# Kernel optimization log

Measured on AMD Instinct MI355X. Metric: run time of the kernel, lower is better.

## Reference

```python
import jax, jax.numpy as jnp
import numpy as np

RANK = 16
ALPHA = 32.0
SCALING = ALPHA / RANK  # 2.0


def setup_inputs() -> dict:
    key = jax.random.key(0)
    k1, k2, k3, k4, k5 = jax.random.split(key, 5)
    B, S, D_IN, D_OUT = 4, 4096, 4096, 4096
    x = jax.random.normal(k1, (B, S, D_IN), dtype=jnp.float32)
    W = jax.random.normal(k2, (D_OUT, D_IN), dtype=jnp.float32) * 0.02
    b = jax.random.normal(k3, (D_OUT,), dtype=jnp.float32) * 0.02
    lora_A = jax.random.normal(k4, (RANK, D_IN), dtype=jnp.float32) * 0.02
    lora_B = jax.random.normal(k5, (D_OUT, RANK), dtype=jnp.float32) * 0.02
    return {"x": x, "W": W, "b": b, "lora_A": lora_A, "lora_B": lora_B}


def reference(x, W, b, lora_A, lora_B):
    # Base linear: y = x @ W^T + b
    base = jnp.einsum("bsd,od->bso", x, W) + b
    # LoRA delta: mathematically x @ (B @ A)^T * scaling == ((x @ A^T) @ B^T) * scaling.
    # We chain the two small rank-limited GEMMs (same math, efficient form).
    xa = jnp.einsum("bsd,rd->bsr", x, lora_A)           # [B,S,rank]
    lora_out = jnp.einsum("bsr,or->bso", xa, lora_B)    # [B,S,out]
    return base + SCALING * lora_out
```

## Files before the change

### kernel.cpp

```cpp
#include <hip/hip_runtime.h>
#include <hip/hip_bf16.h>
#include <cstdint>

constexpr int  KDIM  = 4096;
constexpr int  NDIM  = 4096;
constexpr long MDIM  = 16384;
constexpr int  RANK_ = 16;
constexpr float SCALE_ = 2.0f;

constexpr int BK = 64;
constexpr int NT = KDIM / BK;

using bf16x8 = __attribute__((ext_vector_type(8))) short;
using f32x4  = __attribute__((ext_vector_type(4))) float;

__device__ __forceinline__ void gload_lds16(const void* g, void* l) {
  __builtin_amdgcn_global_load_lds(
      (const __attribute__((address_space(1))) void*)g,
      (__attribute__((address_space(3))) void*)l, 16, 0, 0);
}

__device__ __forceinline__ unsigned short f2bf(float f) {
  union { float f; unsigned u; } v; v.f = f;
  unsigned r = v.u + 0x7FFFu + ((v.u >> 16) & 1u);
  return (unsigned short)(r >> 16);
}

__global__ __launch_bounds__(256) void prep_w_kernel(
    const float* __restrict__ W, const float* __restrict__ lA,
    const float* __restrict__ lB, unsigned short* __restrict__ Wp) {
  const long total8 = (long)NDIM * KDIM / 8;
  for (long t = blockIdx.x * (long)blockDim.x + threadIdx.x; t < total8;
       t += (long)gridDim.x * blockDim.x) {
    const int o  = (int)(t / (KDIM / 8));
    const int d8 = (int)(t % (KDIM / 8)) * 8;
    const float4* w4 = reinterpret_cast<const float4*>(W + (size_t)o * KDIM + d8);
    float4 w0 = w4[0], w1 = w4[1];
    float acc[8] = {w0.x, w0.y, w0.z, w0.w, w1.x, w1.y, w1.z, w1.w};
#pragma unroll
    for (int r = 0; r < RANK_; ++r) {
      const float br = SCALE_ * lB[o * RANK_ + r];
      const float4* a4 = reinterpret_cast<const float4*>(lA + (size_t)r * KDIM + d8);
      float4 a0 = a4[0], a1 = a4[1];
      acc[0] += br * a0.x; acc[1] += br * a0.y; acc[2] += br * a0.z; acc[3] += br * a0.w;
      acc[4] += br * a1.x; acc[5] += br * a1.y; acc[6] += br * a1.z; acc[7] += br * a1.w;
    }
    uint4 o4;
    o4.x = (unsigned)f2bf(acc[0]) | ((unsigned)f2bf(acc[1]) << 16);
    o4.y = (unsigned)f2bf(acc[2]) | ((unsigned)f2bf(acc[3]) << 16);
    o4.z = (unsigned)f2bf(acc[4]) | ((unsigned)f2bf(acc[5]) << 16);
    o4.w = (unsigned)f2bf(acc[6]) | ((unsigned)f2bf(acc[7]) << 16);
    *reinterpret_cast<uint4*>(Wp + t * 8) = o4;
  }
}

__global__ __launch_bounds__(256) void conv_x_kernel(
    const float* __restrict__ x, unsigned short* __restrict__ xb) {
  const long total8 = MDIM * KDIM / 8;
  for (long t = blockIdx.x * (long)blockDim.x + threadIdx.x; t < total8;
       t += (long)gridDim.x * blockDim.x) {
    const float4* p = reinterpret_cast<const float4*>(x + t * 8);
    float4 a = p[0], b = p[1];
    uint4 o4;
    o4.x = (unsigned)f2bf(a.x) | ((unsigned)f2bf(a.y) << 16);
    o4.y = (unsigned)f2bf(a.z) | ((unsigned)f2bf(a.w) << 16);
    o4.z = (unsigned)f2bf(b.x) | ((unsigned)f2bf(b.y) << 16);
    o4.w = (unsigned)f2bf(b.z) | ((unsigned)f2bf(b.w) << 16);
    *reinterpret_cast<uint4*>(xb + t * 8) = o4;
  }
}

__global__ __launch_bounds__(512, 2) void gemm256_kernel(
    const unsigned short* __restrict__ A,
    const unsigned short* __restrict__ Bm,
    const float* __restrict__ bias,
    float* __restrict__ C) {
  __shared__ __align__(16) unsigned char lds[131072];

  const int tid  = threadIdx.x;
  const int wave = tid >> 6, lane = tid & 63;
  const int wm = wave >> 2, wn = wave & 3;
  const int r16 = lane & 15, hi = lane >> 4;
  const int swz5 = ((r16 >> 3) & 1) << 5;
  const int lrB = (wn & 1) * 64;

  const int orig = blockIdx.x;
  const int bid  = (orig & 7) * 128 + (orig >> 3);
  const int bcol = (bid & 15) * 256;
  const int brow = (bid >> 4) * 256;

  const int st_row = wave * 16 + (lane >> 2);
  const int st_col = ((lane & 3) * 8) ^ (((lane >> 5) & 1) << 4);
  const unsigned short* Asrc = A  + (size_t)(brow + st_row) * KDIM + st_col;
  const unsigned short* Bsrc = Bm + (size_t)(bcol + st_row) * KDIM + st_col;

  auto stageHalf = [&](unsigned char* base, int s, int tau) {
    const unsigned short* g = (s >= 2 ? Asrc + (size_t)(s - 2) * 128 * KDIM
                                      : Bsrc + (size_t)s * 128 * KDIM) + tau * BK;
    unsigned char* d = base + (wave << 10) + s * 16384;
    gload_lds16(g,      d);
    gload_lds16(g + 32, d + 8192);
  };

  auto ldfrag = [&](const unsigned char* half, int lrow, int kk) -> bf16x8 {
    return *reinterpret_cast<const bf16x8*>(
        half + kk * 8192 + lrow * 64 + (hi * 16 ^ swz5));
  };

  f32x4 acc[8][4];
#pragma unroll
  for (int m = 0; m < 8; ++m)
#pragma unroll
    for (int n = 0; n < 4; ++n) acc[m][n] = (f32x4){0.f, 0.f, 0.f, 0.f};

  unsigned char* const buf0 = lds;
  unsigned char* const buf1 = lds + 65536;

  stageHalf(buf0, 0, 0); stageHalf(buf0, 1, 0);
  stageHalf(buf0, 2, 0); stageHalf(buf0, 3, 0);
  stageHalf(buf1, 0, 1); stageHalf(buf1, 1, 1);
  asm volatile("s_waitcnt vmcnt(4)" ::: "memory");
  __builtin_amdgcn_s_barrier();

  bf16x8 xlo[4][2], xhi[4][2], wlo[2][2], whi[2][2];

#define KTILE(CUR, NXT, t)                                                     \
  {                                                                            \
    const unsigned char* Ah = (CUR) + (2 + wm) * 16384;                        \
    const unsigned char* Bh = (CUR) + (wn >> 1) * 16384;                       \
           \
    _Pragma("unroll")                                                          \
    for (int n = 0; n < 2; ++n) wlo[n][0] = ldfrag(Bh, lrB + n * 16 + r16, 0); \
    _Pragma("unroll")                                                          \
    for (int m = 0; m < 4; ++m) xlo[m][0] = ldfrag(Ah, m * 16 + r16, 0);       \
    _Pragma("unroll")                                                          \
    for (int n = 0; n < 2; ++n) wlo[n][1] = ldfrag(Bh, lrB + n * 16 + r16, 1); \
    _Pragma("unroll")                                                          \
    for (int m = 0; m < 4; ++m) xlo[m][1] = ldfrag(Ah, m * 16 + r16, 1);       \
    if ((t) + 1 < NT) stageHalf((NXT), 2, (t) + 1);                            \
    asm volatile("s_waitcnt lgkmcnt(8)" ::: "memory");                         \
    __builtin_amdgcn_s_barrier();                                              \
    asm volatile("s_waitcnt lgkmcnt(0)" ::: "memory");                         \
    __builtin_amdgcn_s_setprio(1);                                             \
    _Pragma("unroll")                                                          \
    for (int kk = 0; kk < 2; ++kk)                                             \
      _Pragma("unroll")                                                        \
      for (int m = 0; m < 4; ++m)                                              \
        _Pragma("unroll")                                                      \
        for (int n = 0; n < 2; ++n)                                            \
          acc[m][n] = __builtin_amdgcn_mfma_f32_16x16x32_bf16(                 \
              wlo[n][kk], xlo[m][kk], acc[m][n], 0, 0, 0);                     \
    __builtin_amdgcn_s_setprio(0);                                             \
    __builtin_amdgcn_s_barrier();                                              \
                                 \
    _Pragma("unroll")                                                          \
    for (int n = 0; n < 2; ++n) {                                              \
      whi[n][0] = ldfrag(Bh, lrB + (n + 2) * 16 + r16, 0);                     \
      whi[n][1] = ldfrag(Bh, lrB + (n + 2) * 16 + r16, 1);                     \
    }                                                                          \
    if ((t) + 1 < NT) stageHalf((NXT), 3, (t) + 1);                            \
    __builtin_amdgcn_s_barrier();                                              \
    asm volatile("s_waitcnt lgkmcnt(0)" ::: "memory");                         \
    __builtin_amdgcn_s_setprio(1);                                             \
    _Pragma("unroll")                                                          \
    for (int kk = 0; kk < 2; ++kk)                                             \
      _Pragma("unroll")                                                        \
      for (int m = 0; m < 4; ++m)                                              \
        _Pragma("unroll")                                                      \
        for (int n = 0; n < 2; ++n)                                            \
          acc[m][n + 2] = __builtin_amdgcn_mfma_f32_16x16x32_bf16(             \
              whi[n][kk], xlo[m][kk], acc[m][n + 2], 0, 0, 0);                 \
    __builtin_amdgcn_s_setprio(0);                                             \
    __builtin_amdgcn_s_barrier();                                              \
      \
    _Pragma("unroll")                                                          \
    for (int m = 0; m < 4; ++m) {                                              \
      xhi[m][0] = ldfrag(Ah, (m + 4) * 16 + r16, 0);                           \
      xhi[m][1] = ldfrag(Ah, (m + 4) * 16 + r16, 1);                           \
    }                                                                          \
    if ((t) + 2 < NT) stageHalf((CUR), 0, (t) + 2);                            \
    __builtin_amdgcn_s_barrier();                                              \
    asm volatile("s_waitcnt lgkmcnt(0)" ::: "memory");                         \
    __builtin_amdgcn_s_setprio(1);                                             \
    _Pragma("unroll")                                                          \
    for (int kk = 0; kk < 2; ++kk)                                             \
      _Pragma("unroll")                                                        \
      for (int m = 0; m < 4; ++m)                                              \
        _Pragma("unroll")                                                      \
        for (int n = 0; n < 2; ++n)                                            \
          acc[m + 4][n + 2] = __builtin_amdgcn_mfma_f32_16x16x32_bf16(         \
              whi[n][kk], xhi[m][kk], acc[m + 4][n + 2], 0, 0, 0);             \
    __builtin_amdgcn_s_setprio(0);                                             \
    __builtin_amdgcn_s_barrier();                                              \
               \
    if ((t) + 2 < NT) stageHalf((CUR), 1, (t) + 2);                            \
    __builtin_amdgcn_s_barrier();                                              \
    __builtin_amdgcn_s_setprio(1);                                             \
    _Pragma("unroll")                                                          \
    for (int kk = 0; kk < 2; ++kk)                                             \
      _Pragma("unroll")                                                        \
      for (int m = 0; m < 4; ++m)                                              \
        _Pragma("unroll")                                                      \
        for (int n = 0; n < 2; ++n)                                            \
          acc[m + 4][n] = __builtin_amdgcn_mfma_f32_16x16x32_bf16(             \
              wlo[n][kk], xhi[m][kk], acc[m + 4][n], 0, 0, 0);                 \
    __builtin_amdgcn_s_setprio(0);                                             \
    if ((t) < NT - 2)       asm volatile("s_waitcnt vmcnt(4)" ::: "memory");   \
    else if ((t) == NT - 2) asm volatile("s_waitcnt vmcnt(0)" ::: "memory");   \
    __builtin_amdgcn_s_barrier();                                              \
  }

  for (int tt = 0; tt < NT; tt += 2) {
    KTILE(buf0, buf1, tt);
    KTILE(buf1, buf0, tt + 1);
  }
#undef KTILE

#pragma unroll
  for (int n = 0; n < 4; ++n) {
    const int colb = bcol + wn * 64 + n * 16 + hi * 4;
    const f32x4 bv = *reinterpret_cast<const f32x4*>(&bias[colb]);
#pragma unroll
    for (int m = 0; m < 8; ++m) {
      const size_t row = (size_t)brow + wm * 128 + m * 16 + r16;
      f32x4 v = acc[m][n] + bv;
      *reinterpret_cast<f32x4*>(&C[row * NDIM + colb]) = v;
    }
  }
}

extern "C" void kernel_launch(void* const* d_in, const int* in_sizes, int n_in,
                              void* d_out, int out_size, void* d_ws, size_t ws_size,
                              hipStream_t stream) {
  const float* x  = (const float*)d_in[0];
  const float* W  = (const float*)d_in[1];
  const float* b  = (const float*)d_in[2];
  const float* lA = (const float*)d_in[3];
  const float* lB = (const float*)d_in[4];
  float* out = (float*)d_out;

  unsigned short* xb = (unsigned short*)d_ws;
  unsigned short* Wp = (unsigned short*)((char*)d_ws + (size_t)MDIM * KDIM * 2);

  conv_x_kernel<<<2048, 256, 0, stream>>>(x, xb);
  prep_w_kernel<<<2048, 256, 0, stream>>>(W, lA, lB, Wp);

  gemm256_kernel<<<1024, 512, 0, stream>>>(xb, Wp, b, out);
}
```

Before: 623.1 us.

## Prefetch next tile's A fragments early, drop barriers, swap tile raster order

```diff
diff --git a/kernel.cpp b/kernel.cpp
--- a/kernel.cpp
+++ b/kernel.cpp
@@ -86,8 +86,8 @@
 
   const int orig = blockIdx.x;
   const int bid  = (orig & 7) * 128 + (orig >> 3);
-  const int bcol = (bid & 15) * 256;
-  const int brow = (bid >> 4) * 256;
+  const int brow = (bid & 63) * 256;
+  const int bcol = (bid >> 6) * 256;
 
   const int st_row = wave * 16 + (lane >> 2);
   const int st_col = ((lane & 3) * 8) ^ (((lane >> 5) & 1) << 4);
@@ -122,65 +122,67 @@
   asm volatile("s_waitcnt vmcnt(4)" ::: "memory");
   __builtin_amdgcn_s_barrier();
 
-  bf16x8 xlo[4][2], xhi[4][2], wlo[2][2], whi[2][2];
+  bf16x8 xlo0[4], xlo1[4], xhi[4][2], wlo[2][2], whi[2][2];
+#pragma unroll
+  for (int m = 0; m < 4; ++m)
+    xlo0[m] = ldfrag(buf0 + (2 + wm) * 16384, m * 16 + r16, 0);
 
 #define KTILE(CUR, NXT, t)                                                     \
   {                                                                            \
-    const unsigned char* Ah = (CUR) + (2 + wm) * 16384;                        \
-    const unsigned char* Bh = (CUR) + (wn >> 1) * 16384;                       \
-           \
+    const unsigned char* Ah  = (CUR) + (2 + wm) * 16384;                       \
+    const unsigned char* Bh  = (CUR) + (wn >> 1) * 16384;                      \
+    const unsigned char* AhN = (NXT) + (2 + wm) * 16384;                       \
+                        \
     _Pragma("unroll")                                                          \
     for (int n = 0; n < 2; ++n) wlo[n][0] = ldfrag(Bh, lrB + n * 16 + r16, 0); \
     _Pragma("unroll")                                                          \
-    for (int m = 0; m < 4; ++m) xlo[m][0] = ldfrag(Ah, m * 16 + r16, 0);       \
-    _Pragma("unroll")                                                          \
     for (int n = 0; n < 2; ++n) wlo[n][1] = ldfrag(Bh, lrB + n * 16 + r16, 1); \
     _Pragma("unroll")                                                          \
-    for (int m = 0; m < 4; ++m) xlo[m][1] = ldfrag(Ah, m * 16 + r16, 1);       \
+    for (int m = 0; m < 4; ++m) xlo1[m] = ldfrag(Ah, m * 16 + r16, 1);         \
     if ((t) + 1 < NT) stageHalf((NXT), 2, (t) + 1);                            \
-    asm volatile("s_waitcnt lgkmcnt(8)" ::: "memory");                         \
-    __builtin_amdgcn_s_barrier();                                              \
-    asm volatile("s_waitcnt lgkmcnt(0)" ::: "memory");                         \
-    __builtin_amdgcn_s_setprio(1);                                             \
-    _Pragma("unroll")                                                          \
-    for (int kk = 0; kk < 2; ++kk)                                             \
-      _Pragma("unroll")                                                        \
-      for (int m = 0; m < 4; ++m)                                              \
-        _Pragma("unroll")                                                      \
-        for (int n = 0; n < 2; ++n)                                            \
-          acc[m][n] = __builtin_amdgcn_mfma_f32_16x16x32_bf16(                 \
-              wlo[n][kk], xlo[m][kk], acc[m][n], 0, 0, 0);                     \
-    __builtin_amdgcn_s_setprio(0);                                             \
-    __builtin_amdgcn_s_barrier();                                              \
-                                 \
+    __builtin_amdgcn_s_setprio(1);                                             \
+    _Pragma("unroll")                                                          \
+    for (int m = 0; m < 4; ++m)                                                \
+      _Pragma("unroll")                                                        \
+      for (int n = 0; n < 2; ++n)                                              \
+        acc[m][n] = __builtin_amdgcn_mfma_f32_16x16x32_bf16(                   \
+            wlo[n][0], xlo0[m], acc[m][n], 0, 0, 0);                           \
+    _Pragma("unroll")                                                          \
+    for (int m = 0; m < 4; ++m)                                                \
+      _Pragma("unroll")                                                        \
+      for (int n = 0; n < 2; ++n)                                              \
+        acc[m][n] = __builtin_amdgcn_mfma_f32_16x16x32_bf16(                   \
+            wlo[n][1], xlo1[m], acc[m][n], 0, 0, 0);                           \
+    __builtin_amdgcn_s_setprio(0);                                             \
+    __builtin_amdgcn_s_barrier();                                              \
+                                  \
     _Pragma("unroll")                                                          \
     for (int n = 0; n < 2; ++n) {                                              \
       whi[n][0] = ldfrag(Bh, lrB + (n + 2) * 16 + r16, 0);                     \
       whi[n][1] = ldfrag(Bh, lrB + (n + 2) * 16 + r16, 1);                     \
     }                                                                          \
     if ((t) + 1 < NT) stageHalf((NXT), 3, (t) + 1);                            \
-    __builtin_amdgcn_s_barrier();                                              \
-    asm volatile("s_waitcnt lgkmcnt(0)" ::: "memory");                         \
-    __builtin_amdgcn_s_setprio(1);                                             \
-    _Pragma("unroll")                                                          \
-    for (int kk = 0; kk < 2; ++kk)                                             \
-      _Pragma("unroll")                                                        \
-      for (int m = 0; m < 4; ++m)                                              \
-        _Pragma("unroll")                                                      \
-        for (int n = 0; n < 2; ++n)                                            \
-          acc[m][n + 2] = __builtin_amdgcn_mfma_f32_16x16x32_bf16(             \
-              whi[n][kk], xlo[m][kk], acc[m][n + 2], 0, 0, 0);                 \
-    __builtin_amdgcn_s_setprio(0);                                             \
-    __builtin_amdgcn_s_barrier();                                              \
-      \
-    _Pragma("unroll")                                                          \
-    for (int m = 0; m < 4; ++m) {                                              \
-      xhi[m][0] = ldfrag(Ah, (m + 4) * 16 + r16, 0);                           \
-      xhi[m][1] = ldfrag(Ah, (m + 4) * 16 + r16, 1);                           \
-    }                                                                          \
+    __builtin_amdgcn_s_setprio(1);                                             \
+    _Pragma("unroll")                                                          \
+    for (int m = 0; m < 4; ++m)                                                \
+      _Pragma("unroll")                                                        \
+      for (int n = 0; n < 2; ++n)                                              \
+        acc[m][n + 2] = __builtin_amdgcn_mfma_f32_16x16x32_bf16(               \
+            whi[n][0], xlo0[m], acc[m][n + 2], 0, 0, 0);                       \
+    _Pragma("unroll")                                                          \
+    for (int m = 0; m < 4; ++m)                                                \
+      _Pragma("unroll")                                                        \
+      for (int n = 0; n < 2; ++n)                                              \
+        acc[m][n + 2] = __builtin_amdgcn_mfma_f32_16x16x32_bf16(               \
+            whi[n][1], xlo1[m], acc[m][n + 2], 0, 0, 0);                       \
+    __builtin_amdgcn_s_setprio(0);                                             \
+    __builtin_amdgcn_s_barrier();                                              \
+                         \
+    _Pragma("unroll")                                                          \
+    for (int m = 0; m < 4; ++m) xhi[m][0] = ldfrag(Ah, (m + 4) * 16 + r16, 0); \
+    _Pragma("unroll")                                                          \
+    for (int m = 0; m < 4; ++m) xhi[m][1] = ldfrag(Ah, (m + 4) * 16 + r16, 1); \
     if ((t) + 2 < NT) stageHalf((CUR), 0, (t) + 2);                            \
-    __builtin_amdgcn_s_barrier();                                              \
-    asm volatile("s_waitcnt lgkmcnt(0)" ::: "memory");                         \
     __builtin_amdgcn_s_setprio(1);                                             \
     _Pragma("unroll")                                                          \
     for (int kk = 0; kk < 2; ++kk)                                             \
@@ -192,9 +194,15 @@
               whi[n][kk], xhi[m][kk], acc[m + 4][n + 2], 0, 0, 0);             \
     __builtin_amdgcn_s_setprio(0);                                             \
     __builtin_amdgcn_s_barrier();                                              \
-               \
+          \
     if ((t) + 2 < NT) stageHalf((CUR), 1, (t) + 2);                            \
-    __builtin_amdgcn_s_barrier();                                              \
+    if ((t) < NT - 2)       asm volatile("s_waitcnt vmcnt(4)" ::: "memory");   \
+    else if ((t) == NT - 2) asm volatile("s_waitcnt vmcnt(0)" ::: "memory");   \
+    __builtin_amdgcn_s_barrier();                                              \
+    if ((t) + 1 < NT) {                                                        \
+      _Pragma("unroll")                                                        \
+      for (int m = 0; m < 4; ++m) xlo0[m] = ldfrag(AhN, m * 16 + r16, 0);      \
+    }                                                                          \
     __builtin_amdgcn_s_setprio(1);                                             \
     _Pragma("unroll")                                                          \
     for (int kk = 0; kk < 2; ++kk)                                             \
@@ -205,9 +213,6 @@
           acc[m + 4][n] = __builtin_amdgcn_mfma_f32_16x16x32_bf16(             \
               wlo[n][kk], xhi[m][kk], acc[m + 4][n], 0, 0, 0);                 \
     __builtin_amdgcn_s_setprio(0);                                             \
-    if ((t) < NT - 2)       asm volatile("s_waitcnt vmcnt(4)" ::: "memory");   \
-    else if ((t) == NT - 2) asm volatile("s_waitcnt vmcnt(0)" ::: "memory");   \
-    __builtin_amdgcn_s_barrier();                                              \
   }
 
   for (int tt = 0; tt < NT; tt += 2) {
```

Result: slower. 643.2 us (+3.2%).

## Prefetch LDS fragments one phase ahead and drop intra-tile barriers

Applied to the files above, without the earlier changes.

```diff
diff --git a/kernel.cpp b/kernel.cpp
--- a/kernel.cpp
+++ b/kernel.cpp
@@ -123,24 +123,29 @@
   __builtin_amdgcn_s_barrier();
 
   bf16x8 xlo[4][2], xhi[4][2], wlo[2][2], whi[2][2];
+#pragma unroll
+  for (int m = 0; m < 4; ++m) {
+    xlo[m][0] = ldfrag(buf0 + (2 + wm) * 16384, m * 16 + r16, 0);
+    xlo[m][1] = ldfrag(buf0 + (2 + wm) * 16384, m * 16 + r16, 1);
+  }
 
 #define KTILE(CUR, NXT, t)                                                     \
   {                                                                            \
-    const unsigned char* Ah = (CUR) + (2 + wm) * 16384;                        \
-    const unsigned char* Bh = (CUR) + (wn >> 1) * 16384;                       \
-           \
+    const unsigned char* Ah  = (CUR) + (2 + wm) * 16384;                       \
+    const unsigned char* Bh  = (CUR) + (wn >> 1) * 16384;                      \
+    const unsigned char* AhN = (NXT) + (2 + wm) * 16384;                       \
+       \
     _Pragma("unroll")                                                          \
     for (int n = 0; n < 2; ++n) wlo[n][0] = ldfrag(Bh, lrB + n * 16 + r16, 0); \
     _Pragma("unroll")                                                          \
-    for (int m = 0; m < 4; ++m) xlo[m][0] = ldfrag(Ah, m * 16 + r16, 0);       \
-    _Pragma("unroll")                                                          \
     for (int n = 0; n < 2; ++n) wlo[n][1] = ldfrag(Bh, lrB + n * 16 + r16, 1); \
     _Pragma("unroll")                                                          \
-    for (int m = 0; m < 4; ++m) xlo[m][1] = ldfrag(Ah, m * 16 + r16, 1);       \
+    for (int n = 0; n < 2; ++n)                                                \
+      whi[n][0] = ldfrag(Bh, lrB + (n + 2) * 16 + r16, 0);                     \
+    _Pragma("unroll")                                                          \
+    for (int n = 0; n < 2; ++n)                                                \
+      whi[n][1] = ldfrag(Bh, lrB + (n + 2) * 16 + r16, 1);                     \
     if ((t) + 1 < NT) stageHalf((NXT), 2, (t) + 1);                            \
-    asm volatile("s_waitcnt lgkmcnt(8)" ::: "memory");                         \
-    __builtin_amdgcn_s_barrier();                                              \
-    asm volatile("s_waitcnt lgkmcnt(0)" ::: "memory");                         \
     __builtin_amdgcn_s_setprio(1);                                             \
     _Pragma("unroll")                                                          \
     for (int kk = 0; kk < 2; ++kk)                                             \
@@ -152,15 +157,12 @@
               wlo[n][kk], xlo[m][kk], acc[m][n], 0, 0, 0);                     \
     __builtin_amdgcn_s_setprio(0);                                             \
     __builtin_amdgcn_s_barrier();                                              \
-                                 \
-    _Pragma("unroll")                                                          \
-    for (int n = 0; n < 2; ++n) {                                              \
-      whi[n][0] = ldfrag(Bh, lrB + (n + 2) * 16 + r16, 0);                     \
-      whi[n][1] = ldfrag(Bh, lrB + (n + 2) * 16 + r16, 1);                     \
-    }                                                                          \
+                \
+    _Pragma("unroll")                                                          \
+    for (int m = 0; m < 4; ++m) xhi[m][0] = ldfrag(Ah, (m + 4) * 16 + r16, 0); \
+    _Pragma("unroll")                                                          \
+    for (int m = 0; m < 4; ++m) xhi[m][1] = ldfrag(Ah, (m + 4) * 16 + r16, 1); \
     if ((t) + 1 < NT) stageHalf((NXT), 3, (t) + 1);                            \
-    __builtin_amdgcn_s_barrier();                                              \
-    asm volatile("s_waitcnt lgkmcnt(0)" ::: "memory");                         \
     __builtin_amdgcn_s_setprio(1);                                             \
     _Pragma("unroll")                                                          \
     for (int kk = 0; kk < 2; ++kk)                                             \
@@ -172,15 +174,8 @@
               whi[n][kk], xlo[m][kk], acc[m][n + 2], 0, 0, 0);                 \
     __builtin_amdgcn_s_setprio(0);                                             \
     __builtin_amdgcn_s_barrier();                                              \
-      \
-    _Pragma("unroll")                                                          \
-    for (int m = 0; m < 4; ++m) {                                              \
-      xhi[m][0] = ldfrag(Ah, (m + 4) * 16 + r16, 0);                           \
-      xhi[m][1] = ldfrag(Ah, (m + 4) * 16 + r16, 1);                           \
-    }                                                                          \
+              \
     if ((t) + 2 < NT) stageHalf((CUR), 0, (t) + 2);                            \
-    __builtin_amdgcn_s_barrier();                                              \
-    asm volatile("s_waitcnt lgkmcnt(0)" ::: "memory");                         \
     __builtin_amdgcn_s_setprio(1);                                             \
     _Pragma("unroll")                                                          \
     for (int kk = 0; kk < 2; ++kk)                                             \
@@ -192,9 +187,17 @@
               whi[n][kk], xhi[m][kk], acc[m + 4][n + 2], 0, 0, 0);             \
     __builtin_amdgcn_s_setprio(0);                                             \
     __builtin_amdgcn_s_barrier();                                              \
-               \
+             \
     if ((t) + 2 < NT) stageHalf((CUR), 1, (t) + 2);                            \
-    __builtin_amdgcn_s_barrier();                                              \
+    if ((t) < NT - 2)       asm volatile("s_waitcnt vmcnt(4)" ::: "memory");   \
+    else if ((t) == NT - 2) asm volatile("s_waitcnt vmcnt(0)" ::: "memory");   \
+    __builtin_amdgcn_s_barrier();                                              \
+    if ((t) + 1 < NT) {                                                        \
+      _Pragma("unroll")                                                        \
+      for (int m = 0; m < 4; ++m) xlo[m][0] = ldfrag(AhN, m * 16 + r16, 0);    \
+      _Pragma("unroll")                                                        \
+      for (int m = 0; m < 4; ++m) xlo[m][1] = ldfrag(AhN, m * 16 + r16, 1);    \
+    }                                                                          \
     __builtin_amdgcn_s_setprio(1);                                             \
     _Pragma("unroll")                                                          \
     for (int kk = 0; kk < 2; ++kk)                                             \
@@ -205,9 +208,6 @@
           acc[m + 4][n] = __builtin_amdgcn_mfma_f32_16x16x32_bf16(             \
               wlo[n][kk], xhi[m][kk], acc[m + 4][n], 0, 0, 0);                 \
     __builtin_amdgcn_s_setprio(0);                                             \
-    if ((t) < NT - 2)       asm volatile("s_waitcnt vmcnt(4)" ::: "memory");   \
-    else if ((t) == NT - 2) asm volatile("s_waitcnt vmcnt(0)" ::: "memory");   \
-    __builtin_amdgcn_s_barrier();                                              \
   }
 
   for (int tt = 0; tt < NT; tt += 2) {
```

Measured after the change: 605.1 us. 1.03x faster.
